# Optimization experiments

Hardware: AMD Instinct MI355X
Metric: run time of the kernel (lower is better)

Reference implementation:

```python
import jax, jax.numpy as jnp
import numpy as np

K = 512
D = 256


def setup_inputs() -> dict:
    key = jax.random.key(0)
    k1, k2 = jax.random.split(key)
    z_e = jax.random.normal(k1, (64, D, 32, 32), dtype=jnp.float32)
    # torch init: uniform_(-1/K, 1/K)
    codebook = jax.random.uniform(k2, (K, D), dtype=jnp.float32, minval=-1.0 / K, maxval=1.0 / K)
    return {"z_e": z_e, "codebook": codebook}


def reference(z_e, codebook):
    B, C, H, W = z_e.shape
    # (B,C,H,W) -> (B,H,W,C) -> (N,D)
    z_flat = jnp.transpose(z_e, (0, 2, 3, 1)).reshape(-1, C)
    # squared L2 distances: ||z||^2 + ||e||^2 - 2 z.e  -> [N, K]
    d = (jnp.sum(z_flat ** 2, axis=1, keepdims=True)
         + jnp.sum(codebook ** 2, axis=1)
         - 2.0 * jnp.matmul(z_flat, codebook.T))
    idx = jnp.argmin(d, axis=1)  # [N]
    z_q_flat = codebook[idx]  # [N, D] gather
    z_q = jnp.transpose(z_q_flat.reshape(B, H, W, C), (0, 3, 1, 2))
    commitment_loss = jnp.mean((z_e - jax.lax.stop_gradient(z_q)) ** 2)
    codebook_loss = jnp.mean((z_q - jax.lax.stop_gradient(z_e)) ** 2)
    # straight-through estimator
    z_q_st = z_e + jax.lax.stop_gradient(z_q - z_e)
    indices = idx.reshape(B, H, W)
    return (z_q_st, commitment_loss, codebook_loss, indices)
```

## Files before the change

kernel.cpp:

```cpp
#include <hip/hip_runtime.h>


typedef __attribute__((ext_vector_type(8))) short short8v;
typedef __attribute__((ext_vector_type(4))) float float4v;
typedef unsigned short ushort_t;

namespace {
constexpr int K = 512;
constexpr int D = 256;
constexpr int HW = 1024;
constexpr int NROWS = 65536;
constexpr int CHW = D * HW;

constexpr int ZQ_SIZE = 64 * CHW;
constexpr int LOSS0_OFF = ZQ_SIZE;
constexpr int LOSS1_OFF = ZQ_SIZE + 1;
constexpr int IDX_OFF = ZQ_SIZE + 2;

constexpr int WS_EH_FLOATS = (K * D) / 2;
constexpr int WS_B = WS_EH_FLOATS;
constexpr int WS_KIDX = WS_B + K;
constexpr int WS_PART = WS_KIDX + NROWS;

constexpr int NBLK_A = NROWS / 32;
constexpr int NBLK_G = 2048;

constexpr float EPS_CAND = 3.0e-3f;
constexpr int MAXC = 16;
}

__device__ __forceinline__ ushort_t bf16_rne(float f) {
    unsigned u = __float_as_uint(f);
    u += 0x7fffu + ((u >> 16) & 1u);
    return (ushort_t)(u >> 16);
}

__global__ void vq_prep(const float* __restrict__ cb, float* __restrict__ ws) {
    const int k = blockIdx.x;
    const int t = threadIdx.x;
    ushort_t* eh = (ushort_t*)ws;
    eh[(size_t)k * D + t] = bf16_rne(cb[k * D + t]);
    __shared__ float r16[16];
    if (t < 16) {
#pragma clang fp contract(off)
        const float* x = cb + k * D + (t >> 3) * 128;
        const int j = t & 7;
        float v = x[j];
        float r = v * v;
        for (int i = 1; i < 16; ++i) {
            float w = x[8 * i + j];
            r += w * w;
        }
        r16[t] = r;
    }
    __syncthreads();
    if (t == 0) {
#pragma clang fp contract(off)
        float lo = ((r16[0] + r16[1]) + (r16[2] + r16[3])) +
                   ((r16[4] + r16[5]) + (r16[6] + r16[7]));
        float hi = ((r16[8] + r16[9]) + (r16[10] + r16[11])) +
                   ((r16[12] + r16[13]) + (r16[14] + r16[15]));
        ws[WS_B + k] = lo + hi;
    }
}

__global__ __launch_bounds__(256, 4) void vq_argmin2(
    const float* __restrict__ z_e, const float* __restrict__ cb,
    const ushort_t* __restrict__ eh, const float* __restrict__ Bv,
    int* __restrict__ wsidx, float* __restrict__ out) {
    __shared__ __align__(16) ushort_t zh[32][264];
    __shared__ float lds_B[K];
    __shared__ float scr[32][17];
    __shared__ int cand[32][MAXC];
    __shared__ float lds_A[32];
    __shared__ float wmin[4][32];
    __shared__ float rmin[32];
    __shared__ int cnt[32];

    const int t = threadIdx.x;
    const int row0 = blockIdx.x * 32;
    const int b = row0 >> 10;
    const int hw0 = row0 & 1023;
    const float* zbase = z_e + (size_t)b * CHW + hw0;

    lds_B[t] = Bv[t];
    lds_B[t + 256] = Bv[t + 256];

    {
        const int row = t & 31;
        const int q = t >> 5;
        const int half = q >> 2;
        const int j0 = (q & 3) * 2;
        const int cbase = half * 128;
        const float* zp = zbase + row;
        float r0, r1;
        {
#pragma clang fp contract(off)
            const int c0 = cbase + j0;
            float w0 = zp[(size_t)c0 * HW];
            float w1 = zp[(size_t)(c0 + 1) * HW];
            r0 = w0 * w0;
            r1 = w1 * w1;
            *reinterpret_cast<unsigned*>(&zh[row][c0]) =
                (unsigned)bf16_rne(w0) | ((unsigned)bf16_rne(w1) << 16);
            for (int i = 1; i < 16; ++i) {
                const int c = cbase + 8 * i + j0;
                float u0 = zp[(size_t)c * HW];
                float u1 = zp[(size_t)(c + 1) * HW];
                r0 += u0 * u0;
                r1 += u1 * u1;
                *reinterpret_cast<unsigned*>(&zh[row][c]) =
                    (unsigned)bf16_rne(u0) | ((unsigned)bf16_rne(u1) << 16);
            }
        }
        scr[row][half * 8 + j0] = r0;
        scr[row][half * 8 + j0 + 1] = r1;
    }
    __syncthreads();
    if (t < 32) {
#pragma clang fp contract(off)
        const float* r = scr[t];
        float lo = ((r[0] + r[1]) + (r[2] + r[3])) + ((r[4] + r[5]) + (r[6] + r[7]));
        float hi = ((r[8] + r[9]) + (r[10] + r[11])) + ((r[12] + r[13]) + (r[14] + r[15]));
        lds_A[t] = lo + hi;
    }

    const int lane = t & 63;
    const int w = t >> 6;
    const int wc0 = w * 128;
    const int l15 = lane & 15;
    const int kg = lane >> 4;

    float4v acc[8][2];
#pragma unroll
    for (int c = 0; c < 8; ++c)
#pragma unroll
        for (int rt = 0; rt < 2; ++rt) acc[c][rt] = (float4v)0.f;

    const ushort_t* ehp = eh + (size_t)(wc0 + l15) * D + 8 * kg;

#pragma unroll 4
    for (int d0 = 0; d0 < D; d0 += 32) {
        const short8v bh0 = *reinterpret_cast<const short8v*>(&zh[l15][d0 + 8 * kg]);
        const short8v bh1 = *reinterpret_cast<const short8v*>(&zh[16 + l15][d0 + 8 * kg]);
#pragma unroll
        for (int c = 0; c < 8; ++c) {
            const short8v a = *reinterpret_cast<const short8v*>(ehp + c * 16 * D + d0);
            acc[c][0] = __builtin_amdgcn_mfma_f32_16x16x32_bf16(a, bh0, acc[c][0], 0, 0, 0);
            acc[c][1] = __builtin_amdgcn_mfma_f32_16x16x32_bf16(a, bh1, acc[c][1], 0, 0, 0);
        }
    }
    __syncthreads();

    float lmin0 = 3.0e38f, lmin1 = 3.0e38f;
#pragma unroll
    for (int c = 0; c < 8; ++c)
#pragma unroll
        for (int rt = 0; rt < 2; ++rt)
#pragma unroll
            for (int r = 0; r < 4; ++r) {
                const int code = wc0 + 16 * c + 4 * kg + r;
                const int row = rt * 16 + l15;
                float s = (lds_A[row] + lds_B[code]) - 2.0f * acc[c][rt][r];
                acc[c][rt][r] = s;
                if (rt == 0) lmin0 = fminf(lmin0, s);
                else lmin1 = fminf(lmin1, s);
            }
    lmin0 = fminf(lmin0, __shfl_xor(lmin0, 16));
    lmin0 = fminf(lmin0, __shfl_xor(lmin0, 32));
    lmin1 = fminf(lmin1, __shfl_xor(lmin1, 16));
    lmin1 = fminf(lmin1, __shfl_xor(lmin1, 32));
    if (lane < 16) {
        wmin[w][l15] = lmin0;
        wmin[w][16 + l15] = lmin1;
    }
    __syncthreads();
    if (t < 32) {
        rmin[t] = fminf(fminf(wmin[0][t], wmin[1][t]), fminf(wmin[2][t], wmin[3][t]));
        cnt[t] = 0;
    }
    __syncthreads();

#pragma unroll
    for (int c = 0; c < 8; ++c)
#pragma unroll
        for (int rt = 0; rt < 2; ++rt) {
            const int row = rt * 16 + l15;
            const float thr = rmin[row] + EPS_CAND;
#pragma unroll
            for (int r = 0; r < 4; ++r) {
                if (acc[c][rt][r] <= thr) {
                    const int code = wc0 + 16 * c + 4 * kg + r;
                    int slot = atomicAdd(&cnt[row], 1);
                    if (slot < MAXC) cand[row][slot] = code;
                }
            }
        }
    __syncthreads();

    float* ed = reinterpret_cast<float*>(&zh[0][0]);
    int* ek = reinterpret_cast<int*>(ed + 256);
    {
        const int row = t & 31;
        const int ct = t >> 5;
        const float* zp = zbase + row;
        const int n = cnt[row];
        float bd = 3.0e38f;
        int bk = 0x7fffffff;
        if (n == 1) {
            if (ct == 0) {
                bd = -3.0e38f;
                bk = cand[row][0];
            }
        } else {
            const bool full = (n > MAXC);
            const int lim = full ? K : n;
            for (int s = ct; s < lim; s += 8) {
                const int k = full ? s : cand[row][s];
                const float* ep = cb + (size_t)k * D;
                float a = 0.f;
#pragma unroll 8
                for (int c = 0; c < D; ++c) a = fmaf(zp[(size_t)c * HW], ep[c], a);
                float dv;
                {
#pragma clang fp contract(off)
                    float t1 = lds_A[row] + lds_B[k];
                    dv = t1 - 2.0f * a;
                }
                if (dv < bd || (dv == bd && k < bk)) {
                    bd = dv;
                    bk = k;
                }
            }
        }
        ed[t] = bd;
        ek[t] = bk;
    }
    __syncthreads();
    if (t < 32) {
        float bd = ed[t];
        int bk = ek[t];
#pragma unroll
        for (int q = 1; q < 8; ++q) {
            float od = ed[q * 32 + t];
            int ok = ek[q * 32 + t];
            if (od < bd || (od == bd && ok < bk)) {
                bd = od;
                bk = ok;
            }
        }
        wsidx[row0 + t] = bk;
        out[IDX_OFF + row0 + t] = (float)bk;
    }
}

__global__ __launch_bounds__(256, 8) void vq_gather2(
    const float* __restrict__ z_e, const float* __restrict__ cb,
    const int* __restrict__ wsidx, float* __restrict__ part,
    float* __restrict__ out) {
    __shared__ float wpart[4];
    const int t = threadIdx.x;
    const int blk = blockIdx.x;
    const int cg = blk & 7;
    const int q = (blk >> 3) & 3;
    const int b = blk >> 5;
    const int lane = t & 63;
    const int csub = t >> 6;
    const int hw = q * 256 + lane * 4;

    const int4 kk = *reinterpret_cast<const int4*>(&wsidx[b * HW + hw]);
    const float* e0 = cb + (size_t)kk.x * D;
    const float* e1 = cb + (size_t)kk.y * D;
    const float* e2 = cb + (size_t)kk.z * D;
    const float* e3 = cb + (size_t)kk.w * D;
    const size_t zoff = (size_t)b * CHW + hw;

    float accum = 0.f;
#pragma unroll 2
    for (int i = 0; i < 8; ++i) {
        const int c = cg * 32 + csub * 8 + i;
        const size_t off = zoff + (size_t)c * HW;
        const float4 z4 = *reinterpret_cast<const float4*>(&z_e[off]);
        const float ex = e0[c], ey = e1[c], ez = e2[c], ew = e3[c];
        float4 o4;
        o4.x = z4.x + (ex - z4.x);
        o4.y = z4.y + (ey - z4.y);
        o4.z = z4.z + (ez - z4.z);
        o4.w = z4.w + (ew - z4.w);
        *reinterpret_cast<float4*>(&out[off]) = o4;
        accum = fmaf(z4.x - ex, z4.x - ex, accum);
        accum = fmaf(z4.y - ey, z4.y - ey, accum);
        accum = fmaf(z4.z - ez, z4.z - ez, accum);
        accum = fmaf(z4.w - ew, z4.w - ew, accum);
    }
#pragma unroll
    for (int m = 1; m < 64; m <<= 1) accum += __shfl_xor(accum, m);
    if (lane == 0) wpart[csub] = accum;
    __syncthreads();
    if (t == 0) part[blk] = (wpart[0] + wpart[1]) + (wpart[2] + wpart[3]);
}

__global__ void vq_finish(const float* __restrict__ part, float* __restrict__ out) {
    const int t = threadIdx.x;
    double s = 0.0;
#pragma unroll
    for (int i = 0; i < 8; ++i) s += (double)part[t + 256 * i];
#pragma unroll
    for (int m = 1; m < 64; m <<= 1) s += __shfl_xor(s, m);
    __shared__ double wsum[4];
    if ((t & 63) == 0) wsum[t >> 6] = s;
    __syncthreads();
    if (t == 0) {
        double mean = (wsum[0] + wsum[1] + wsum[2] + wsum[3]) / (double)ZQ_SIZE;
        out[LOSS0_OFF] = (float)mean;
        out[LOSS1_OFF] = (float)mean;
    }
}

extern "C" void kernel_launch(void* const* d_in, const int* in_sizes, int n_in,
                              void* d_out, int out_size, void* d_ws, size_t ws_size,
                              hipStream_t stream) {
    const float* z_e = (const float*)d_in[0];
    const float* cb = (const float*)d_in[1];
    float* out = (float*)d_out;
    float* ws = (float*)d_ws;

    const ushort_t* eh = (const ushort_t*)ws;
    float* Bv = ws + WS_B;
    int* wsidx = (int*)(ws + WS_KIDX);
    float* part = ws + WS_PART;

    vq_prep<<<K, D, 0, stream>>>(cb, ws);
    vq_argmin2<<<NBLK_A, 256, 0, stream>>>(z_e, cb, eh, Bv, wsidx, out);
    vq_gather2<<<NBLK_G, 256, 0, stream>>>(z_e, cb, wsidx, part, out);
    vq_finish<<<1, 256, 0, stream>>>(part, out);
}
```

Measured before the change: 148.4 us.

## Move exact argmin refinement into a separate compacted work-queue kernel

Rows left ambiguous by the bf16 MFMA pass are no longer refined inside the argmin block. They are appended to a global queue via ballot and an atomic counter, and a new kernel then refines each one with a single wavefront and shuffle-based reductions. Rows with a single candidate write their index directly. This removes the block-wide stall where all 256 threads wait on a few rows needing fp32 dot products, and it trims the argmin kernel's tail. In exchange it adds a kernel launch, global traffic for the row norms and candidate lists, and a smaller candidate cap, so more rows fall back to a full 512-code scan.

```diff
diff --git a/kernel.cpp b/kernel.cpp
--- a/kernel.cpp
+++ b/kernel.cpp
@@ -19,14 +19,19 @@
 
 constexpr int WS_EH_FLOATS = (K * D) / 2;
 constexpr int WS_B = WS_EH_FLOATS;
-constexpr int WS_KIDX = WS_B + K;
+constexpr int WS_A = WS_B + K;
+constexpr int WS_KIDX = WS_A + NROWS;
 constexpr int WS_PART = WS_KIDX + NROWS;
+constexpr int WS_PCNT = WS_PART + 2048;
+constexpr int WS_PMETA = WS_PCNT + 4;
+constexpr int WS_PCAND = WS_PMETA + NROWS;
 
 constexpr int NBLK_A = NROWS / 32;
 constexpr int NBLK_G = 2048;
+constexpr int NBLK_E = 1024;
 
 constexpr float EPS_CAND = 3.0e-3f;
-constexpr int MAXC = 16;
+constexpr int MAXC = 8;
 }
 
 __device__ __forceinline__ ushort_t bf16_rne(float f) {
@@ -38,6 +43,7 @@
 __global__ void vq_prep(const float* __restrict__ cb, float* __restrict__ ws) {
     const int k = blockIdx.x;
     const int t = threadIdx.x;
+    if (k == 0 && t == 0) reinterpret_cast<int*>(ws + WS_PCNT)[0] = 0;
     ushort_t* eh = (ushort_t*)ws;
     eh[(size_t)k * D + t] = bf16_rne(cb[k * D + t]);
     __shared__ float r16[16];
@@ -64,10 +70,12 @@
     }
 }
 
-__global__ __launch_bounds__(256, 4) void vq_argmin2(
-    const float* __restrict__ z_e, const float* __restrict__ cb,
-    const ushort_t* __restrict__ eh, const float* __restrict__ Bv,
-    int* __restrict__ wsidx, float* __restrict__ out) {
+__global__ __launch_bounds__(256, 4) void vq_argmin3(
+    const float* __restrict__ z_e, const ushort_t* __restrict__ eh,
+    const float* __restrict__ Bv, float* __restrict__ wsA,
+    int* __restrict__ gpcnt, unsigned* __restrict__ pmeta,
+    ushort_t* __restrict__ pcand, int* __restrict__ wsidx,
+    float* __restrict__ out) {
     __shared__ __align__(16) ushort_t zh[32][264];
     __shared__ float lds_B[K];
     __shared__ float scr[32][17];
@@ -123,6 +131,7 @@
         float lo = ((r[0] + r[1]) + (r[2] + r[3])) + ((r[4] + r[5]) + (r[6] + r[7]));
         float hi = ((r[8] + r[9]) + (r[10] + r[11])) + ((r[12] + r[13]) + (r[14] + r[15]));
         lds_A[t] = lo + hi;
+        wsA[row0 + t] = lo + hi;
     }
 
     const int lane = t & 63;
@@ -198,33 +207,79 @@
         }
     __syncthreads();
 
-    float* ed = reinterpret_cast<float*>(&zh[0][0]);
-    int* ek = reinterpret_cast<int*>(ed + 256);
-    {
-        const int row = t & 31;
-        const int ct = t >> 5;
-        const float* zp = zbase + row;
-        const int n = cnt[row];
+    if (t < 64) {
+        const int n = (t < 32) ? cnt[t] : 0;
+        const bool pend = (t < 32) && (n >= 2);
+        const unsigned long long m = __ballot(pend);
+        int base = 0;
+        if (t == 0 && m != 0ull) base = atomicAdd(gpcnt, __popcll(m));
+        base = __shfl(base, 0);
+        if (t < 32) {
+            if (n == 1) {
+                const int bk = cand[t][0];
+                wsidx[row0 + t] = bk;
+                out[IDX_OFF + row0 + t] = (float)bk;
+            } else {
+                const int slot = base + __popcll(m & ((1ull << t) - 1ull));
+                pmeta[slot] = (unsigned)(row0 + t) | ((unsigned)n << 16);
+                const int ns = (n < MAXC) ? n : MAXC;
+                for (int j = 0; j < ns; ++j)
+                    pcand[(size_t)slot * MAXC + j] = (ushort_t)cand[t][j];
+            }
+        }
+    }
+}
+
+__global__ __launch_bounds__(256) void vq_exact(
+    const float* __restrict__ z_e, const float* __restrict__ cb,
+    const float* __restrict__ Bv, const float* __restrict__ wsA,
+    const unsigned* __restrict__ pmeta, const ushort_t* __restrict__ pcand,
+    const int* __restrict__ gpcnt, int* __restrict__ wsidx,
+    float* __restrict__ out) {
+    __shared__ float zx[4][260];
+    const int t = threadIdx.x;
+    const int wv = t >> 6;
+    const int lane = t & 63;
+    const int nw = gridDim.x * 4;
+    const int total = *gpcnt;
+
+    for (int slot = blockIdx.x * 4 + wv; slot < total; slot += nw) {
+        const unsigned mt = pmeta[slot];
+        const int r = mt & 0xFFFFu;
+        const int n = (int)(mt >> 16);
+        const int b = r >> 10;
+        const int hw = r & 1023;
+        const float* zp = z_e + (size_t)b * CHW + hw;
+#pragma unroll
+        for (int i = 0; i < 4; ++i)
+            zx[wv][lane + 64 * i] = zp[(size_t)(lane + 64 * i) * HW];
+        const float aval = wsA[r];
         float bd = 3.0e38f;
         int bk = 0x7fffffff;
-        if (n == 1) {
-            if (ct == 0) {
-                bd = -3.0e38f;
-                bk = cand[row][0];
-            }
-        } else {
-            const bool full = (n > MAXC);
-            const int lim = full ? K : n;
-            for (int s = ct; s < lim; s += 8) {
-                const int k = full ? s : cand[row][s];
+        if (n <= MAXC) {
+            if (lane < n) {
+                const int k = pcand[(size_t)slot * MAXC + lane];
                 const float* ep = cb + (size_t)k * D;
                 float a = 0.f;
 #pragma unroll 8
-                for (int c = 0; c < D; ++c) a = fmaf(zp[(size_t)c * HW], ep[c], a);
+                for (int c = 0; c < D; ++c) a = fmaf(zx[wv][c], ep[c], a);
+                {
+#pragma clang fp contract(off)
+                    float t1 = aval + Bv[k];
+                    bd = t1 - 2.0f * a;
+                }
+                bk = k;
+            }
+        } else {
+            for (int k = lane; k < K; k += 64) {
+                const float* ep = cb + (size_t)k * D;
+                float a = 0.f;
+#pragma unroll 8
+                for (int c = 0; c < D; ++c) a = fmaf(zx[wv][c], ep[c], a);
                 float dv;
                 {
 #pragma clang fp contract(off)
-                    float t1 = lds_A[row] + lds_B[k];
+                    float t1 = aval + Bv[k];
                     dv = t1 - 2.0f * a;
                 }
                 if (dv < bd || (dv == bd && k < bk)) {
@@ -233,24 +288,19 @@
                 }
             }
         }
-        ed[t] = bd;
-        ek[t] = bk;
-    }
-    __syncthreads();
-    if (t < 32) {
-        float bd = ed[t];
-        int bk = ek[t];
-#pragma unroll
-        for (int q = 1; q < 8; ++q) {
-            float od = ed[q * 32 + t];
-            int ok = ek[q * 32 + t];
+#pragma unroll
+        for (int m = 1; m < 64; m <<= 1) {
+            float od = __shfl_xor(bd, m);
+            int ok = __shfl_xor(bk, m);
             if (od < bd || (od == bd && ok < bk)) {
                 bd = od;
                 bk = ok;
             }
         }
-        wsidx[row0 + t] = bk;
-        out[IDX_OFF + row0 + t] = (float)bk;
+        if (lane == 0) {
+            wsidx[r] = bk;
+            out[IDX_OFF + r] = (float)bk;
+        }
     }
 }
 
@@ -327,11 +377,18 @@
 
     const ushort_t* eh = (const ushort_t*)ws;
     float* Bv = ws + WS_B;
+    float* wsA = ws + WS_A;
     int* wsidx = (int*)(ws + WS_KIDX);
     float* part = ws + WS_PART;
+    int* gpcnt = (int*)(ws + WS_PCNT);
+    unsigned* pmeta = (unsigned*)(ws + WS_PMETA);
+    ushort_t* pcand = (ushort_t*)(ws + WS_PCAND);
 
     vq_prep<<<K, D, 0, stream>>>(cb, ws);
-    vq_argmin2<<<NBLK_A, 256, 0, stream>>>(z_e, cb, eh, Bv, wsidx, out);
+    vq_argmin3<<<NBLK_A, 256, 0, stream>>>(z_e, eh, Bv, wsA, gpcnt, pmeta,
+                                           pcand, wsidx, out);
+    vq_exact<<<NBLK_E, 256, 0, stream>>>(z_e, cb, Bv, wsA, pmeta, pcand,
+                                         gpcnt, wsidx, out);
     vq_gather2<<<NBLK_G, 256, 0, stream>>>(z_e, cb, wsidx, part, out);
     vq_finish<<<1, 256, 0, stream>>>(part, out);
 }
```

Measured after the change: 202.6 us. 36.6% more time.
